# Kernel tuning notes

Measured on AMD Instinct MI355X. Metric: run time of the kernel, lower is better.

Reference implementation:

```python
import jax, jax.numpy as jnp
import numpy as np

EPS = 1e-5

@jax.custom_vjp
def ste_sign(x):
    # Binarize: sign(x); backward is straight-through identity (BNN convention)
    return jnp.sign(x)

def _ste_fwd(x):
    return jnp.sign(x), None

def _ste_bwd(_, g):
    return (g,)

ste_sign.defvjp(_ste_fwd, _ste_bwd)

def bn(y, gamma, beta, mean, var):
    # inference-mode BatchNorm2d over channel axis 1
    inv = gamma * jax.lax.rsqrt(var + EPS)
    return y * inv[None, :, None, None] + (beta - mean * inv)[None, :, None, None]

def setup_inputs() -> dict:
    key = jax.random.key(0)
    ks = jax.random.split(key, 11)
    B, C, H, W = 32, 256, 56, 56
    return {
        "x":  jax.random.normal(ks[0], (B, C, H, W), jnp.float32),
        "w1": jax.random.normal(ks[1], (3 * C, C), jnp.float32),   # 1x1 conv kernel [out,in]
        "w2": jax.random.normal(ks[2], (C, 3 * C), jnp.float32),
        "g1": jax.random.uniform(ks[3], (3 * C,), jnp.float32, 0.5, 1.5),
        "b1": jax.random.normal(ks[4], (3 * C,), jnp.float32),
        "m1": jax.random.normal(ks[5], (3 * C,), jnp.float32),
        "v1": jax.random.uniform(ks[6], (3 * C,), jnp.float32, 0.5, 1.5),
        "g2": jax.random.uniform(ks[7], (C,), jnp.float32, 0.5, 1.5),
        "b2": jax.random.normal(ks[8], (C,), jnp.float32),
        "m2": jax.random.normal(ks[9], (C,), jnp.float32),
        "v2": jax.random.uniform(ks[10], (C,), jnp.float32, 0.5, 1.5),
    }

def reference(x, w1, w2, g1, b1, m1, v1, g2, b2, m2, v2):
    # BinarizeConv2d: binarize input + weight, 1x1 conv == channel GEMM
    y1 = jnp.einsum('oc,bchw->bohw', ste_sign(w1), ste_sign(x))
    y1 = bn(y1, g1, b1, m1, v1)
    y2 = jnp.einsum('oc,bchw->bohw', ste_sign(w2), ste_sign(y1))
    y2 = bn(y2, g2, b2, m2, v2)
    return y2 + x
```

## Files before the change

kernel.cpp:

```cpp
#include <hip/hip_runtime.h>

typedef unsigned long long u64;
typedef int i32x4 __attribute__((ext_vector_type(4)));

#define HW    3136
#define CIN   256
#define CMID  768
#define EPSV  1e-5

__global__ __launch_bounds__(64) void prep_kernel(
    const float* __restrict__ w1, const float* __restrict__ w2,
    const float* __restrict__ g1, const float* __restrict__ b1,
    const float* __restrict__ m1, const float* __restrict__ v1,
    const float* __restrict__ g2, const float* __restrict__ b2,
    const float* __restrict__ m2, const float* __restrict__ v2,
    char* __restrict__ w1t, char* __restrict__ w2t,
    float2* __restrict__ ic1, float2* __restrict__ ic2)
{
  int blk = blockIdx.x, lane = threadIdx.x;
  if (blk < 384) {
    const float* src;
    char* dst;
    int row, k0, ldk;
    if (blk < 192) {
      int rt = blk >> 2, kt = blk & 3;
      row = rt * 16 + (lane & 15);
      k0  = kt * 64 + (lane >> 4) * 16;
      src = w1; ldk = 256; dst = w1t + (size_t)blk * 1024;
    } else {
      int tid = blk - 192;
      int rt = tid / 12, kt = tid - rt * 12;
      row = rt * 16 + (lane & 15);
      k0  = kt * 64 + (lane >> 4) * 16;
      src = w2; ldk = 768; dst = w2t + (size_t)tid * 1024;
    }
    const float* sp = src + (size_t)row * ldk + k0;
    unsigned d[4];
    #pragma unroll
    for (int q = 0; q < 4; ++q) {
      unsigned dv = 0;
      #pragma unroll
      for (int j = 0; j < 4; ++j) {
        float v = sp[q * 4 + j];
        unsigned s = (v < 0.f) ? 0xFFu : (v > 0.f ? 1u : 0u);
        dv |= s << (8 * j);
      }
      d[q] = dv;
    }
    i32x4 vv; vv.x = (int)d[0]; vv.y = (int)d[1]; vv.z = (int)d[2]; vv.w = (int)d[3];
    *(i32x4*)(dst + lane * 16) = vv;
  } else {
    int i = (blk - 384) * 64 + lane;
    if (i < CMID) {
      double inv = (double)g1[i] / sqrt((double)v1[i] + EPSV);
      float2 o; o.x = (float)inv;
      o.y = (float)((double)b1[i] - (double)m1[i] * inv);
      ic1[i] = o;
    } else if (i < CMID + CIN) {
      int j = i - CMID;
      double inv = (double)g2[j] / sqrt((double)v2[j] + EPSV);
      float2 o; o.x = (float)inv;
      o.y = (float)((double)b2[j] - (double)m2[j] * inv);
      ic2[j] = o;
    }
  }
}

__global__ __launch_bounds__(256, 2) void bnn_kernel(
    const float* __restrict__ x,
    const char* __restrict__ w1t, const char* __restrict__ w2t,
    const float2* __restrict__ ic1, const float2* __restrict__ ic2,
    float* __restrict__ out)
{
  __shared__ __align__(16) char sBx[64 * 256];
  __shared__ __align__(16) char sY[64 * 768];

  int t    = threadIdx.x;
  int w    = t >> 6;
  int lane = t & 63;
  int l15  = lane & 15;
  int g4   = lane >> 4;
  int swz  = l15 << 4;
  int lb   = lane << 4;

  int px0 = blockIdx.x * 64;
  int b   = px0 / HW;
  int hw0 = px0 - b * HW;
  const float* xb = x   + (size_t)b * (CIN * HW) + hw0;
  float*       ob = out + (size_t)b * (CIN * HW) + hw0;

  {
    const float* xp = xb + lane + (size_t)(w << 6) * HW;
    int rowbase = lane * 256 + (w << 6);
    int pswz    = (lane & 15) << 4;
    #pragma unroll
    for (int j = 0; j < 4; ++j) {
      unsigned d[4];
      #pragma unroll
      for (int q = 0; q < 4; ++q) {
        unsigned dv = 0;
        #pragma unroll
        for (int bb = 0; bb < 4; ++bb) {
          int c = j * 16 + q * 4 + bb;
          unsigned u = __float_as_uint(xp[(size_t)c * HW]);
          unsigned s = ((u + u) == 0u) ? 0u : (((int)u < 0) ? 0xFFu : 1u);
          dv |= s << (8 * bb);
        }
        d[q] = dv;
      }
      i32x4 v; v.x = (int)d[0]; v.y = (int)d[1]; v.z = (int)d[2]; v.w = (int)d[3];
      *(i32x4*)&sBx[(rowbase + j * 16) ^ pswz] = v;
    }
  }
  __syncthreads();

  i32x4 bfa[4][4];
  #pragma unroll
  for (int ks = 0; ks < 4; ++ks) {
    int k0 = ks * 64 + g4 * 16;
    #pragma unroll
    for (int n = 0; n < 4; ++n)
      bfa[ks][n] = *(const i32x4*)&sBx[((n * 16 + l15) * 256 + k0) ^ swz];
  }

  #pragma unroll 1
  for (int ch = 0; ch < 4; ++ch) {
    int rt0 = w * 12 + ch * 3;
    i32x4 acc[3][4];
    #pragma unroll
    for (int m = 0; m < 3; ++m)
      #pragma unroll
      for (int n = 0; n < 4; ++n) acc[m][n] = (i32x4)0;

    #pragma unroll
    for (int ks = 0; ks < 4; ++ks) {
      i32x4 af[3];
      #pragma unroll
      for (int m = 0; m < 3; ++m)
        af[m] = *(const i32x4*)&w1t[(size_t)((rt0 + m) * 4 + ks) * 1024 + lb];
      #pragma unroll
      for (int m = 0; m < 3; ++m)
        #pragma unroll
        for (int n = 0; n < 4; ++n)
          acc[m][n] = __builtin_amdgcn_mfma_i32_16x16x64_i8(
              af[m], bfa[ks][n], acc[m][n], 0, 0, 0);
    }

    #pragma unroll
    for (int m = 0; m < 3; ++m) {
      int r0 = (rt0 + m) * 16 + g4 * 4;
      float2 c0 = ic1[r0], c1 = ic1[r0 + 1], c2 = ic1[r0 + 2], c3 = ic1[r0 + 3];
      #pragma unroll
      for (int n = 0; n < 4; ++n) {
        int px = n * 16 + l15;
        float y0 = fmaf((float)acc[m][n].x, c0.x, c0.y);
        float y1 = fmaf((float)acc[m][n].y, c1.x, c1.y);
        float y2 = fmaf((float)acc[m][n].z, c2.x, c2.y);
        float y3 = fmaf((float)acc[m][n].w, c3.x, c3.y);
        unsigned dv =
            (unsigned)(y0 < 0.f ? 0xFFu : (y0 > 0.f ? 1u : 0u))
          | ((unsigned)(y1 < 0.f ? 0xFFu : (y1 > 0.f ? 1u : 0u)) << 8)
          | ((unsigned)(y2 < 0.f ? 0xFFu : (y2 > 0.f ? 1u : 0u)) << 16)
          | ((unsigned)(y3 < 0.f ? 0xFFu : (y3 > 0.f ? 1u : 0u)) << 24);
        *(unsigned*)&sY[(px * 768 + r0) ^ swz] = dv;
      }
    }
  }
  __syncthreads();

  {
    int rbase = w << 6;
    i32x4 acc[4][4];
    #pragma unroll
    for (int m = 0; m < 4; ++m)
      #pragma unroll
      for (int n = 0; n < 4; ++n) acc[m][n] = (i32x4)0;

    #pragma unroll 4
    for (int ks = 0; ks < 12; ++ks) {
      int k0 = ks * 64 + g4 * 16;
      i32x4 bf[4];
      #pragma unroll
      for (int n = 0; n < 4; ++n)
        bf[n] = *(const i32x4*)&sY[((n * 16 + l15) * 768 + k0) ^ swz];
      i32x4 af[4];
      #pragma unroll
      for (int m = 0; m < 4; ++m)
        af[m] = *(const i32x4*)&w2t[(size_t)((w * 4 + m) * 12 + ks) * 1024 + lb];
      #pragma unroll
      for (int m = 0; m < 4; ++m)
        #pragma unroll
        for (int n = 0; n < 4; ++n)
          acc[m][n] = __builtin_amdgcn_mfma_i32_16x16x64_i8(
              af[m], bf[n], acc[m][n], 0, 0, 0);
    }

    #pragma unroll
    for (int m = 0; m < 4; ++m) {
      int r0 = rbase + m * 16 + g4 * 4;
      float2 c0 = ic2[r0], c1 = ic2[r0 + 1], c2 = ic2[r0 + 2], c3 = ic2[r0 + 3];
      #pragma unroll
      for (int n = 0; n < 4; ++n) {
        int pxo = n * 16 + l15;
        const float* xq = xb + pxo;
        float*       oq = ob + pxo;
        size_t o0 = (size_t)r0 * HW;
        oq[o0]          = fmaf((float)acc[m][n].x, c0.x, c0.y) + xq[o0];
        oq[o0 + HW]     = fmaf((float)acc[m][n].y, c1.x, c1.y) + xq[o0 + HW];
        oq[o0 + 2 * HW] = fmaf((float)acc[m][n].z, c2.x, c2.y) + xq[o0 + 2 * HW];
        oq[o0 + 3 * HW] = fmaf((float)acc[m][n].w, c3.x, c3.y) + xq[o0 + 3 * HW];
      }
    }
  }
}

extern "C" void kernel_launch(void* const* d_in, const int* in_sizes, int n_in,
                              void* d_out, int out_size, void* d_ws, size_t ws_size,
                              hipStream_t stream) {
  const float* x  = (const float*)d_in[0];
  const float* w1 = (const float*)d_in[1];
  const float* w2 = (const float*)d_in[2];
  const float* g1 = (const float*)d_in[3];
  const float* b1 = (const float*)d_in[4];
  const float* m1 = (const float*)d_in[5];
  const float* v1 = (const float*)d_in[6];
  const float* g2 = (const float*)d_in[7];
  const float* b2 = (const float*)d_in[8];
  const float* m2 = (const float*)d_in[9];
  const float* v2 = (const float*)d_in[10];
  float* out = (float*)d_out;

  char*   w1t = (char*)d_ws;
  char*   w2t = w1t + 196608;
  float2* ic1 = (float2*)(w2t + 196608);
  float2* ic2 = ic1 + CMID;

  prep_kernel<<<400, 64, 0, stream>>>(w1, w2, g1, b1, m1, v1,
                                      g2, b2, m2, v2, w1t, w2t, ic1, ic2);
  bnn_kernel<<<1568, 256, 0, stream>>>(x, w1t, w2t, ic1, ic2, out);
}
```

Baseline: 108.4 us.

## Split pixel tile into two halves and overlap x loads with GEMM stages

After: 129.3 us. +19.3%, slower.

```diff
diff --git a/kernel.cpp b/kernel.cpp
--- a/kernel.cpp
+++ b/kernel.cpp
@@ -66,14 +66,15 @@
   }
 }
 
-__global__ __launch_bounds__(256, 2) void bnn_kernel(
+__global__ __launch_bounds__(256, 4) void bnn_kernel(
     const float* __restrict__ x,
     const char* __restrict__ w1t, const char* __restrict__ w2t,
     const float2* __restrict__ ic1, const float2* __restrict__ ic2,
     float* __restrict__ out)
 {
-  __shared__ __align__(16) char sBx[64 * 256];
-  __shared__ __align__(16) char sY[64 * 768];
+  __shared__ __align__(16) char sBxA[32 * 256];
+  __shared__ __align__(16) char sBxB[32 * 256];
+  __shared__ __align__(16) char sY[32 * 768];
 
   int t    = threadIdx.x;
   int w    = t >> 6;
@@ -89,129 +90,131 @@
   const float* xb = x   + (size_t)b * (CIN * HW) + hw0;
   float*       ob = out + (size_t)b * (CIN * HW) + hw0;
 
-  {
-    const float* xp = xb + lane + (size_t)(w << 6) * HW;
-    int rowbase = lane * 256 + (w << 6);
-    int pswz    = (lane & 15) << 4;
-    #pragma unroll
-    for (int j = 0; j < 4; ++j) {
-      unsigned d[4];
-      #pragma unroll
-      for (int q = 0; q < 4; ++q) {
-        unsigned dv = 0;
-        #pragma unroll
-        for (int bb = 0; bb < 4; ++bb) {
-          int c = j * 16 + q * 4 + bb;
-          unsigned u = __float_as_uint(xp[(size_t)c * HW]);
-          unsigned s = ((u + u) == 0u) ? 0u : (((int)u < 0) ? 0xFFu : 1u);
-          dv |= s << (8 * bb);
-        }
-        d[q] = dv;
-      }
-      i32x4 v; v.x = (int)d[0]; v.y = (int)d[1]; v.z = (int)d[2]; v.w = (int)d[3];
-      *(i32x4*)&sBx[(rowbase + j * 16) ^ pswz] = v;
-    }
-  }
-  __syncthreads();
-
-  i32x4 bfa[4][4];
-  #pragma unroll
-  for (int ks = 0; ks < 4; ++ks) {
-    int k0 = ks * 64 + g4 * 16;
-    #pragma unroll
-    for (int n = 0; n < 4; ++n)
-      bfa[ks][n] = *(const i32x4*)&sBx[((n * 16 + l15) * 256 + k0) ^ swz];
-  }
-
-  #pragma unroll 1
-  for (int ch = 0; ch < 4; ++ch) {
-    int rt0 = w * 12 + ch * 3;
-    i32x4 acc[3][4];
-    #pragma unroll
-    for (int m = 0; m < 3; ++m)
-      #pragma unroll
-      for (int n = 0; n < 4; ++n) acc[m][n] = (i32x4)0;
-
-    #pragma unroll
-    for (int ks = 0; ks < 4; ++ks) {
-      i32x4 af[3];
-      #pragma unroll
-      for (int m = 0; m < 3; ++m)
-        af[m] = *(const i32x4*)&w1t[(size_t)((rt0 + m) * 4 + ks) * 1024 + lb];
-      #pragma unroll
-      for (int m = 0; m < 3; ++m)
-        #pragma unroll
-        for (int n = 0; n < 4; ++n)
-          acc[m][n] = __builtin_amdgcn_mfma_i32_16x16x64_i8(
-              af[m], bfa[ks][n], acc[m][n], 0, 0, 0);
-    }
-
-    #pragma unroll
-    for (int m = 0; m < 3; ++m) {
-      int r0 = (rt0 + m) * 16 + g4 * 4;
-      float2 c0 = ic1[r0], c1 = ic1[r0 + 1], c2 = ic1[r0 + 2], c3 = ic1[r0 + 3];
-      #pragma unroll
-      for (int n = 0; n < 4; ++n) {
-        int px = n * 16 + l15;
-        float y0 = fmaf((float)acc[m][n].x, c0.x, c0.y);
-        float y1 = fmaf((float)acc[m][n].y, c1.x, c1.y);
-        float y2 = fmaf((float)acc[m][n].z, c2.x, c2.y);
-        float y3 = fmaf((float)acc[m][n].w, c3.x, c3.y);
-        unsigned dv =
-            (unsigned)(y0 < 0.f ? 0xFFu : (y0 > 0.f ? 1u : 0u))
-          | ((unsigned)(y1 < 0.f ? 0xFFu : (y1 > 0.f ? 1u : 0u)) << 8)
-          | ((unsigned)(y2 < 0.f ? 0xFFu : (y2 > 0.f ? 1u : 0u)) << 16)
-          | ((unsigned)(y3 < 0.f ? 0xFFu : (y3 > 0.f ? 1u : 0u)) << 24);
-        *(unsigned*)&sY[(px * 768 + r0) ^ swz] = dv;
-      }
-    }
-  }
-  __syncthreads();
-
-  {
-    int rbase = w << 6;
-    i32x4 acc[4][4];
-    #pragma unroll
-    for (int m = 0; m < 4; ++m)
-      #pragma unroll
-      for (int n = 0; n < 4; ++n) acc[m][n] = (i32x4)0;
-
-    #pragma unroll 4
-    for (int ks = 0; ks < 12; ++ks) {
-      int k0 = ks * 64 + g4 * 16;
-      i32x4 bf[4];
-      #pragma unroll
-      for (int n = 0; n < 4; ++n)
-        bf[n] = *(const i32x4*)&sY[((n * 16 + l15) * 768 + k0) ^ swz];
-      i32x4 af[4];
-      #pragma unroll
-      for (int m = 0; m < 4; ++m)
-        af[m] = *(const i32x4*)&w2t[(size_t)((w * 4 + m) * 12 + ks) * 1024 + lb];
-      #pragma unroll
-      for (int m = 0; m < 4; ++m)
-        #pragma unroll
-        for (int n = 0; n < 4; ++n)
-          acc[m][n] = __builtin_amdgcn_mfma_i32_16x16x64_i8(
-              af[m], bf[n], acc[m][n], 0, 0, 0);
-    }
-
-    #pragma unroll
-    for (int m = 0; m < 4; ++m) {
-      int r0 = rbase + m * 16 + g4 * 4;
-      float2 c0 = ic2[r0], c1 = ic2[r0 + 1], c2 = ic2[r0 + 2], c3 = ic2[r0 + 3];
-      #pragma unroll
-      for (int n = 0; n < 4; ++n) {
-        int pxo = n * 16 + l15;
-        const float* xq = xb + pxo;
-        float*       oq = ob + pxo;
-        size_t o0 = (size_t)r0 * HW;
-        oq[o0]          = fmaf((float)acc[m][n].x, c0.x, c0.y) + xq[o0];
-        oq[o0 + HW]     = fmaf((float)acc[m][n].y, c1.x, c1.y) + xq[o0 + HW];
-        oq[o0 + 2 * HW] = fmaf((float)acc[m][n].z, c2.x, c2.y) + xq[o0 + 2 * HW];
-        oq[o0 + 3 * HW] = fmaf((float)acc[m][n].w, c3.x, c3.y) + xq[o0 + 3 * HW];
-      }
-    }
-  }
+  int p  = t & 31;
+  int h  = t >> 5;
+  int pswz = (p & 15) << 4;
+
+#define PACK_LOAD(XR, TOFF)                                                   \
+  {                                                                           \
+    const float* xp = xb + (p + (TOFF)) + (size_t)(h << 5) * HW;              \
+    _Pragma("unroll") for (int c = 0; c < 32; ++c)                            \
+      XR[c] = xp[(size_t)c * HW];                                             \
+  }
+
+#define PACK_SIGN(XR, SBX)                                                    \
+  {                                                                           \
+    int rowbase = p * 256 + (h << 5);                                         \
+    _Pragma("unroll") for (int j = 0; j < 2; ++j) {                           \
+      unsigned d[4];                                                          \
+      _Pragma("unroll") for (int q = 0; q < 4; ++q) {                         \
+        unsigned dv = 0;                                                      \
+        _Pragma("unroll") for (int bb = 0; bb < 4; ++bb) {                    \
+          unsigned u = __float_as_uint(XR[j * 16 + q * 4 + bb]);              \
+          unsigned s = ((u + u) == 0u) ? 0u : (((int)u < 0) ? 0xFFu : 1u);    \
+          dv |= s << (8 * bb);                                                \
+        }                                                                     \
+        d[q] = dv;                                                            \
+      }                                                                       \
+      i32x4 v; v.x = (int)d[0]; v.y = (int)d[1]; v.z = (int)d[2]; v.w = (int)d[3]; \
+      *(i32x4*)&SBX[(rowbase + j * 16) ^ pswz] = v;                           \
+    }                                                                         \
+  }
+
+#define L1T(SBX)                                                              \
+  _Pragma("unroll 1") for (int ch = 0; ch < 4; ++ch) {                        \
+    int rt0 = w * 12 + ch * 3;                                                \
+    i32x4 acc[3][2];                                                          \
+    _Pragma("unroll") for (int m = 0; m < 3; ++m)                             \
+    _Pragma("unroll") for (int n = 0; n < 2; ++n) acc[m][n] = (i32x4)0;       \
+    _Pragma("unroll") for (int ks = 0; ks < 4; ++ks) {                        \
+      int k0 = ks * 64 + g4 * 16;                                             \
+      i32x4 bf[2];                                                            \
+      _Pragma("unroll") for (int n = 0; n < 2; ++n)                           \
+        bf[n] = *(const i32x4*)&SBX[((n * 16 + l15) * 256 + k0) ^ swz];       \
+      i32x4 af[3];                                                            \
+      _Pragma("unroll") for (int m = 0; m < 3; ++m)                           \
+        af[m] = *(const i32x4*)&w1t[(size_t)((rt0 + m) * 4 + ks) * 1024 + lb];\
+      _Pragma("unroll") for (int m = 0; m < 3; ++m)                           \
+      _Pragma("unroll") for (int n = 0; n < 2; ++n)                           \
+        acc[m][n] = __builtin_amdgcn_mfma_i32_16x16x64_i8(                    \
+            af[m], bf[n], acc[m][n], 0, 0, 0);                                \
+    }                                                                         \
+    _Pragma("unroll") for (int m = 0; m < 3; ++m) {                           \
+      int r0 = (rt0 + m) * 16 + g4 * 4;                                       \
+      float2 c0 = ic1[r0], c1 = ic1[r0+1], c2 = ic1[r0+2], c3 = ic1[r0+3];    \
+      _Pragma("unroll") for (int n = 0; n < 2; ++n) {                         \
+        int px = n * 16 + l15;                                                \
+        float y0 = fmaf((float)acc[m][n].x, c0.x, c0.y);                      \
+        float y1 = fmaf((float)acc[m][n].y, c1.x, c1.y);                      \
+        float y2 = fmaf((float)acc[m][n].z, c2.x, c2.y);                      \
+        float y3 = fmaf((float)acc[m][n].w, c3.x, c3.y);                      \
+        unsigned dv =                                                         \
+            (unsigned)(y0 < 0.f ? 0xFFu : (y0 > 0.f ? 1u : 0u))               \
+          | ((unsigned)(y1 < 0.f ? 0xFFu : (y1 > 0.f ? 1u : 0u)) << 8)        \
+          | ((unsigned)(y2 < 0.f ? 0xFFu : (y2 > 0.f ? 1u : 0u)) << 16)       \
+          | ((unsigned)(y3 < 0.f ? 0xFFu : (y3 > 0.f ? 1u : 0u)) << 24);      \
+        *(unsigned*)&sY[(px * 768 + r0) ^ swz] = dv;                          \
+      }                                                                       \
+    }                                                                         \
+  }
+
+#define L2T(TOFF)                                                             \
+  {                                                                           \
+    int rbase = w << 6;                                                       \
+    i32x4 acc[4][2];                                                          \
+    _Pragma("unroll") for (int m = 0; m < 4; ++m)                             \
+    _Pragma("unroll") for (int n = 0; n < 2; ++n) acc[m][n] = (i32x4)0;       \
+    _Pragma("unroll 4") for (int ks = 0; ks < 12; ++ks) {                     \
+      int k0 = ks * 64 + g4 * 16;                                             \
+      i32x4 bf[2];                                                            \
+      _Pragma("unroll") for (int n = 0; n < 2; ++n)                           \
+        bf[n] = *(const i32x4*)&sY[((n * 16 + l15) * 768 + k0) ^ swz];        \
+      i32x4 af[4];                                                            \
+      _Pragma("unroll") for (int m = 0; m < 4; ++m)                           \
+        af[m] = *(const i32x4*)&w2t[(size_t)((w * 4 + m) * 12 + ks) * 1024 + lb]; \
+      _Pragma("unroll") for (int m = 0; m < 4; ++m)                           \
+      _Pragma("unroll") for (int n = 0; n < 2; ++n)                           \
+        acc[m][n] = __builtin_amdgcn_mfma_i32_16x16x64_i8(                    \
+            af[m], bf[n], acc[m][n], 0, 0, 0);                                \
+    }                                                                         \
+    _Pragma("unroll") for (int m = 0; m < 4; ++m) {                           \
+      int r0 = (w << 6) + m * 16 + g4 * 4;                                    \
+      float2 c0 = ic2[r0], c1 = ic2[r0+1], c2 = ic2[r0+2], c3 = ic2[r0+3];    \
+      _Pragma("unroll") for (int n = 0; n < 2; ++n) {                         \
+        int pxo = n * 16 + l15 + (TOFF);                                      \
+        const float* xq = xb + pxo;                                           \
+        float*       oq = ob + pxo;                                           \
+        size_t o0 = (size_t)r0 * HW;                                          \
+        oq[o0]          = fmaf((float)acc[m][n].x, c0.x, c0.y) + xq[o0];      \
+        oq[o0 + HW]     = fmaf((float)acc[m][n].y, c1.x, c1.y) + xq[o0 + HW]; \
+        oq[o0 + 2*HW]   = fmaf((float)acc[m][n].z, c2.x, c2.y) + xq[o0 + 2*HW]; \
+        oq[o0 + 3*HW]   = fmaf((float)acc[m][n].w, c3.x, c3.y) + xq[o0 + 3*HW]; \
+      }                                                                       \
+    }                                                                         \
+  }
+
+  float xrA[32], xrB[32];
+  PACK_LOAD(xrA, 0);
+  PACK_SIGN(xrA, sBxA);
+  __syncthreads();
+
+  PACK_LOAD(xrB, 32);
+  L1T(sBxA);
+  __syncthreads();
+
+  PACK_SIGN(xrB, sBxB);
+  L2T(0);
+  __syncthreads();
+
+  L1T(sBxB);
+  __syncthreads();
+
+  L2T(32);
+
+#undef PACK_LOAD
+#undef PACK_SIGN
+#undef L1T
+#undef L2T
 }
 
 extern "C" void kernel_launch(void* const* d_in, const int* in_sizes, int n_in,
```

## Split fused BNN kernel into two stages with bit-packed intermediate activations

Applied to the files above, without the earlier changes.

New measurement: 151.6 us. +39.9%, slower.

```diff
diff --git a/kernel.cpp b/kernel.cpp
--- a/kernel.cpp
+++ b/kernel.cpp
@@ -7,6 +7,24 @@
 #define CIN   256
 #define CMID  768
 #define EPSV  1e-5
+
+__device__ __forceinline__ u64 shfl_xor64(u64 v, int m) {
+  unsigned lo = (unsigned)__shfl_xor((int)(unsigned)v, m);
+  unsigned hi = (unsigned)__shfl_xor((int)(v >> 32), m);
+  return ((u64)hi << 32) | lo;
+}
+
+__device__ __forceinline__ i32x4 unpack16(unsigned bits) {
+  i32x4 r;
+  #pragma unroll
+  for (int q = 0; q < 4; ++q) {
+    unsigned nib    = (bits >> (4 * q)) & 0xFu;
+    unsigned spread = (nib * 0x00204081u) & 0x01010101u;
+    unsigned d      = 0x01010101u ^ ((spread << 8) - (spread << 1));
+    r[q] = (int)d;
+  }
+  return r;
+}
 
 __global__ __launch_bounds__(64) void prep_kernel(
     const float* __restrict__ w1, const float* __restrict__ w2,
@@ -66,7 +84,193 @@
   }
 }
 
-__global__ __launch_bounds__(256, 2) void bnn_kernel(
+__global__ __launch_bounds__(256, 4) void l1_kernel(
+    const float* __restrict__ x, const char* __restrict__ w1t,
+    const float2* __restrict__ ic1, u64* __restrict__ gsy)
+{
+  __shared__ __align__(16) char sBx[64 * 256];
+
+  int t    = threadIdx.x;
+  int w    = t >> 6;
+  int lane = t & 63;
+  int l15  = lane & 15;
+  int g4   = lane >> 4;
+  int swz  = l15 << 4;
+  int lb   = lane << 4;
+
+  int px0 = blockIdx.x * 64;
+  int b   = px0 / HW;
+  int hw0 = px0 - b * HW;
+  const float* xb = x + (size_t)b * (CIN * HW) + hw0;
+
+  {
+    const float* xp = xb + lane + (size_t)(w << 6) * HW;
+    int rowbase = lane * 256 + (w << 6);
+    int pswz    = (lane & 15) << 4;
+    #pragma unroll
+    for (int j = 0; j < 4; ++j) {
+      unsigned d[4];
+      #pragma unroll
+      for (int q = 0; q < 4; ++q) {
+        unsigned dv = 0;
+        #pragma unroll
+        for (int bb = 0; bb < 4; ++bb) {
+          int c = j * 16 + q * 4 + bb;
+          unsigned u = __float_as_uint(xp[(size_t)c * HW]);
+          unsigned s = ((u + u) == 0u) ? 0u : (((int)u < 0) ? 0xFFu : 1u);
+          dv |= s << (8 * bb);
+        }
+        d[q] = dv;
+      }
+      i32x4 v; v.x = (int)d[0]; v.y = (int)d[1]; v.z = (int)d[2]; v.w = (int)d[3];
+      *(i32x4*)&sBx[(rowbase + j * 16) ^ pswz] = v;
+    }
+  }
+  __syncthreads();
+
+  u64 syb[4][3];
+  #pragma unroll
+  for (int n = 0; n < 4; ++n)
+    #pragma unroll
+    for (int j = 0; j < 3; ++j) syb[n][j] = 0ull;
+
+  #pragma unroll 1
+  for (int ch = 0; ch < 6; ++ch) {
+    int rt0 = w * 12 + ch * 2;
+    i32x4 acc[2][4];
+    #pragma unroll
+    for (int m = 0; m < 2; ++m)
+      #pragma unroll
+      for (int n = 0; n < 4; ++n) acc[m][n] = (i32x4)0;
+
+    #pragma unroll
+    for (int ks = 0; ks < 4; ++ks) {
+      int k0 = ks * 64 + g4 * 16;
+      i32x4 bf[4];
+      #pragma unroll
+      for (int n = 0; n < 4; ++n)
+        bf[n] = *(const i32x4*)&sBx[((n * 16 + l15) * 256 + k0) ^ swz];
+      i32x4 af[2];
+      #pragma unroll
+      for (int m = 0; m < 2; ++m)
+        af[m] = *(const i32x4*)&w1t[(size_t)((rt0 + m) * 4 + ks) * 1024 + lb];
+      #pragma unroll
+      for (int m = 0; m < 2; ++m)
+        #pragma unroll
+        for (int n = 0; n < 4; ++n)
+          acc[m][n] = __builtin_amdgcn_mfma_i32_16x16x64_i8(
+              af[m], bf[n], acc[m][n], 0, 0, 0);
+    }
+
+    #pragma unroll
+    for (int m = 0; m < 2; ++m) {
+      int base = ch * 32 + m * 16;
+      int wd   = base >> 6;
+      int bo   = base & 63;
+      int r0   = w * 192 + base + g4 * 4;
+      float2 c0 = ic1[r0], c1 = ic1[r0 + 1], c2 = ic1[r0 + 2], c3 = ic1[r0 + 3];
+      #pragma unroll
+      for (int n = 0; n < 4; ++n) {
+        float y0 = fmaf((float)acc[m][n].x, c0.x, c0.y);
+        float y1 = fmaf((float)acc[m][n].y, c1.x, c1.y);
+        float y2 = fmaf((float)acc[m][n].z, c2.x, c2.y);
+        float y3 = fmaf((float)acc[m][n].w, c3.x, c3.y);
+        unsigned nib = (y0 < 0.f ? 1u : 0u) | (y1 < 0.f ? 2u : 0u)
+                     | (y2 < 0.f ? 4u : 0u) | (y3 < 0.f ? 8u : 0u);
+        syb[n][wd] |= (u64)nib << (bo + g4 * 4);
+      }
+    }
+  }
+
+  #pragma unroll
+  for (int n = 0; n < 4; ++n)
+    #pragma unroll
+    for (int j = 0; j < 3; ++j) {
+      u64 v = syb[n][j];
+      v |= shfl_xor64(v, 16);
+      v |= shfl_xor64(v, 32);
+      syb[n][j] = v;
+    }
+  if (g4 < 3) {
+    #pragma unroll
+    for (int n = 0; n < 4; ++n)
+      gsy[(size_t)(px0 + n * 16 + l15) * 12 + 3 * w + g4] = syb[n][g4];
+  }
+}
+
+__global__ __launch_bounds__(256, 4) void l2_kernel(
+    const float* __restrict__ x, const char* __restrict__ w2t,
+    const float2* __restrict__ ic2, const u64* __restrict__ gsy,
+    float* __restrict__ out)
+{
+  __shared__ u64 ssy[64][13];
+
+  int t    = threadIdx.x;
+  int w    = t >> 6;
+  int lane = t & 63;
+  int l15  = lane & 15;
+  int g4   = lane >> 4;
+  int lb   = lane << 4;
+
+  int px0 = blockIdx.x * 64;
+  int b   = px0 / HW;
+  int hw0 = px0 - b * HW;
+  const float* xb = x   + (size_t)b * (CIN * HW) + hw0;
+  float*       ob = out + (size_t)b * (CIN * HW) + hw0;
+
+  for (int i = t; i < 768; i += 256) {
+    int px = i / 12;
+    ssy[px][i - px * 12] = gsy[(size_t)px0 * 12 + i];
+  }
+  __syncthreads();
+
+  int rbase = w << 6;
+  i32x4 acc[4][4];
+  #pragma unroll
+  for (int m = 0; m < 4; ++m)
+    #pragma unroll
+    for (int n = 0; n < 4; ++n) acc[m][n] = (i32x4)0;
+
+  #pragma unroll 4
+  for (int ks = 0; ks < 12; ++ks) {
+    i32x4 bf[4];
+    #pragma unroll
+    for (int n = 0; n < 4; ++n) {
+      u64 wv = ssy[n * 16 + l15][ks];
+      unsigned bits = (unsigned)(wv >> (g4 * 16)) & 0xFFFFu;
+      bf[n] = unpack16(bits);
+    }
+    i32x4 af[4];
+    #pragma unroll
+    for (int m = 0; m < 4; ++m)
+      af[m] = *(const i32x4*)&w2t[(size_t)((w * 4 + m) * 12 + ks) * 1024 + lb];
+    #pragma unroll
+    for (int m = 0; m < 4; ++m)
+      #pragma unroll
+      for (int n = 0; n < 4; ++n)
+        acc[m][n] = __builtin_amdgcn_mfma_i32_16x16x64_i8(
+            af[m], bf[n], acc[m][n], 0, 0, 0);
+  }
+
+  #pragma unroll
+  for (int m = 0; m < 4; ++m) {
+    int r0 = rbase + m * 16 + g4 * 4;
+    float2 c0 = ic2[r0], c1 = ic2[r0 + 1], c2 = ic2[r0 + 2], c3 = ic2[r0 + 3];
+    #pragma unroll
+    for (int n = 0; n < 4; ++n) {
+      int pxo = n * 16 + l15;
+      const float* xq = xb + pxo;
+      float*       oq = ob + pxo;
+      size_t o0 = (size_t)r0 * HW;
+      oq[o0]          = fmaf((float)acc[m][n].x, c0.x, c0.y) + xq[o0];
+      oq[o0 + HW]     = fmaf((float)acc[m][n].y, c1.x, c1.y) + xq[o0 + HW];
+      oq[o0 + 2 * HW] = fmaf((float)acc[m][n].z, c2.x, c2.y) + xq[o0 + 2 * HW];
+      oq[o0 + 3 * HW] = fmaf((float)acc[m][n].w, c3.x, c3.y) + xq[o0 + 3 * HW];
+    }
+  }
+}
+
+__global__ __launch_bounds__(256, 2) void bnn_fused_kernel(
     const float* __restrict__ x,
     const char* __restrict__ w1t, const char* __restrict__ w2t,
     const float2* __restrict__ ic1, const float2* __restrict__ ic2,
@@ -234,8 +438,16 @@
   char*   w2t = w1t + 196608;
   float2* ic1 = (float2*)(w2t + 196608);
   float2* ic2 = ic1 + CMID;
+  u64*    gsy = (u64*)(ic2 + CIN);
 
   prep_kernel<<<400, 64, 0, stream>>>(w1, w2, g1, b1, m1, v1,
                                       g2, b2, m2, v2, w1t, w2t, ic1, ic2);
-  bnn_kernel<<<1568, 256, 0, stream>>>(x, w1t, w2t, ic1, ic2, out);
-}
+
+  size_t need = 196608u * 2 + 8192u + (size_t)100352 * 12 * 8;
+  if (ws_size >= need) {
+    l1_kernel<<<1568, 256, 0, stream>>>(x, w1t, ic1, gsy);
+    l2_kernel<<<1568, 256, 0, stream>>>(x, w2t, ic2, gsy, out);
+  } else {
+    bnn_fused_kernel<<<1568, 256, 0, stream>>>(x, w1t, w2t, ic1, ic2, out);
+  }
+}
```
